# Performance work log

Hardware: AMD Instinct MI355X
Metric: run time of the kernel (lower is better)

The kernel has to match this reference:

```python
import jax, jax.numpy as jnp
import numpy as np

_B = 8      # number of graphs in batch
_H = 8      # attention heads
_GH = 64    # ProteinGraphConvModule output_dim / GRU hidden


def _custom_conv(x, src, dst, lw, lb, qw, qb, kw, kb, vw, vb, abias):
    # Per-edge multi-head attention: softmax is over the head axis within each edge
    n = x.shape[0]
    x = x @ lw + lb
    d = x.shape[1] // _H
    q = (x[dst] @ qw + qb).reshape(-1, _H, d)   # x_i = target nodes
    k = (x[src] @ kw + kb).reshape(-1, _H, d)   # x_j = source nodes
    v = (x[src] @ vw + vb).reshape(-1, _H, d)
    s = jnp.einsum('ehd,egd->ehg', q, k) * (1.0 / d ** 0.5) + abias[..., None]  # (E,H,H)
    a = jax.nn.softmax(s, axis=-1)
    out = jnp.einsum('ehg,egd->ehd', a, v).reshape(-1, _H * d)
    return jax.ops.segment_sum(out, dst, num_segments=n)  # aggr='add'


def _gcn(x, src, dst, w, b):
    # GCNConv: add self-loops + symmetric normalization
    n = x.shape[0]
    loop = jnp.arange(n)
    s = jnp.concatenate([src, loop])
    t = jnp.concatenate([dst, loop])
    deg = jax.ops.segment_sum(jnp.ones(s.shape[0], x.dtype), t, num_segments=n)
    dis = jnp.where(deg > 0, 1.0 / jnp.sqrt(deg), 0.0)
    h = x @ w
    msg = h[s] * (dis[s] * dis[t])[:, None]
    return jax.ops.segment_sum(msg, t, num_segments=n) + b


def _segment_mean(x, seg, nseg):
    ssum = jax.ops.segment_sum(x, seg, num_segments=nseg)
    cnt = jax.ops.segment_sum(jnp.ones(x.shape[0], x.dtype), seg, num_segments=nseg)
    return ssum / jnp.maximum(cnt, 1.0)[:, None]


def _pos_encoding(n, dim):
    pos = np.arange(n, dtype=np.float32)[:, None]
    div = np.exp(np.arange(0, dim, 2, dtype=np.float32) * (-np.log(10000.0) / dim))
    pe = np.zeros((n, dim), np.float32)
    pe[:, 0::2] = np.sin(pos * div)
    pe[:, 1::2] = np.cos(pos * div)
    return jnp.asarray(pe)


def _forward(x_wt, x_diff, emb_w, emb_b, cw_lin_w, cw_lin_b, cw_q_w, cw_q_b, cw_k_w, cw_k_b, cw_v_w, cw_v_b, cw_bias, c3_lin_w, c3_lin_b, c3_q_w, c3_q_b, c3_k_w, c3_k_b, c3_v_w, c3_v_b, c3_bias, sft_w, sft_b, gru_wih, gru_whh, gru_bih, gru_bhh, gcn_w1, gcn_b1, gcn_w2, gcn_b2, gcn_w3, gcn_b3, mlp_w1, mlp_b1, mlp_w2, mlp_b2, mlp_w3, mlp_b3, pred_w, pred_b, edge_index_wt, edge_index_diff, batch_wt, batch_diff):
    sw, dw = edge_index_wt[0], edge_index_wt[1]
    sd, dd = edge_index_diff[0], edge_index_diff[1]

    # ---- ProteinGraphConvModule ----
    x = jax.nn.relu(x_wt @ emb_w + emb_b)
    for i in range(2):  # GNN_depth-1 hidden CustomConvs
        x = jax.nn.relu(_custom_conv(x, sw, dw, cw_lin_w[i], cw_lin_b[i], cw_q_w[i], cw_q_b[i], cw_k_w[i], cw_k_b[i], cw_v_w[i], cw_v_b[i], cw_bias[i]))
    x = jax.nn.relu(_custom_conv(x, sw, dw, c3_lin_w, c3_lin_b, c3_q_w, c3_q_b, c3_k_w, c3_k_b, c3_v_w, c3_v_b, c3_bias))  # (N, 64)

    sf = _segment_mean(x, batch_wt, _B)
    sf = jax.nn.relu(sf @ sft_w + sft_b)
    # GRUCell with h0 = 0 (vectorized over batch)
    gi = sf @ gru_wih.T + gru_bih
    gh = jnp.zeros_like(sf) @ gru_whh.T + gru_bhh
    r = jax.nn.sigmoid(gi[:, :_GH] + gh[:, :_GH])
    z = jax.nn.sigmoid(gi[:, _GH:2 * _GH] + gh[:, _GH:2 * _GH])
    ng = jnp.tanh(gi[:, 2 * _GH:] + r * gh[:, 2 * _GH:])
    sf = (1.0 - z) * ng  # + z * h0 (h0=0)

    x = x + _pos_encoding(x.shape[0], _GH)
    vf_wt = jnp.concatenate([x, sf[batch_wt]], axis=1)  # (N, 128)

    # ---- DiffGraphGNN (eval mode: dropout = identity) ----
    y = jax.nn.relu(_gcn(x_diff, sd, dd, gcn_w1, gcn_b1))
    y = jax.nn.relu(_gcn(y, sd, dd, gcn_w2, gcn_b2))
    vf_diff = _gcn(y, sd, dd, gcn_w3, gcn_b3)  # (N, 128)

    # ---- Pool + MLP head ----
    g_wt = _segment_mean(vf_wt, batch_wt, _B)
    g_diff = _segment_mean(vf_diff, batch_diff, _B)
    h = jnp.concatenate([g_wt, g_diff], axis=-1)  # (B, 256)
    h = jax.nn.relu(h @ mlp_w1 + mlp_b1)
    h = jax.nn.relu(h @ mlp_w2 + mlp_b2)
    h = h @ mlp_w3 + mlp_b3
    return (h @ pred_w + pred_b).squeeze(-1)  # (B,)


def setup_inputs() -> dict:
    key = jax.random.key(0)
    ks = jax.random.split(key, 48)
    N, E, NF, HID = 6000, 200000, 64, 256
    inp = {}
    inp['x_wt'] = jax.random.normal(ks[0], (N, NF), jnp.float32)
    inp['x_diff'] = jax.random.normal(ks[1], (N, NF), jnp.float32)
    inp['edge_index_wt'] = jax.random.randint(ks[2], (2, E), 0, N)
    inp['edge_index_diff'] = jax.random.randint(ks[3], (2, E), 0, N)
    inp['batch_wt'] = jnp.sort(jax.random.randint(ks[4], (N,), 0, _B))
    inp['batch_diff'] = jnp.sort(jax.random.randint(ks[5], (N,), 0, _B))
    shapes = dict(
        emb_w=(NF, HID), emb_b=(HID,),
        cw_lin_w=(2, HID, HID), cw_lin_b=(2, HID), cw_q_w=(2, HID, HID), cw_q_b=(2, HID),
        cw_k_w=(2, HID, HID), cw_k_b=(2, HID), cw_v_w=(2, HID, HID), cw_v_b=(2, HID), cw_bias=(2, 1, _H),
        c3_lin_w=(HID, _GH), c3_lin_b=(_GH,), c3_q_w=(_GH, _GH), c3_q_b=(_GH,),
        c3_k_w=(_GH, _GH), c3_k_b=(_GH,), c3_v_w=(_GH, _GH), c3_v_b=(_GH,), c3_bias=(1, _H),
        sft_w=(_GH, _GH), sft_b=(_GH,),
        gru_wih=(3 * _GH, _GH), gru_whh=(3 * _GH, _GH), gru_bih=(3 * _GH,), gru_bhh=(3 * _GH,),
        gcn_w1=(NF, HID), gcn_b1=(HID,), gcn_w2=(HID, HID), gcn_b2=(HID,), gcn_w3=(HID, 128), gcn_b3=(128,),
        mlp_w1=(256, 128), mlp_b1=(128,), mlp_w2=(128, 128), mlp_b2=(128,), mlp_w3=(128, 128), mlp_b3=(128,),
        pred_w=(128, 1), pred_b=(1,))
    for j, (name, shp) in enumerate(shapes.items()):
        inp[name] = jax.random.normal(ks[6 + j], shp, jnp.float32) * 0.05
    return inp


def reference(x_wt, x_diff, emb_w, emb_b, cw_lin_w, cw_lin_b, cw_q_w, cw_q_b, cw_k_w, cw_k_b, cw_v_w, cw_v_b, cw_bias, c3_lin_w, c3_lin_b, c3_q_w, c3_q_b, c3_k_w, c3_k_b, c3_v_w, c3_v_b, c3_bias, sft_w, sft_b, gru_wih, gru_whh, gru_bih, gru_bhh, gcn_w1, gcn_b1, gcn_w2, gcn_b2, gcn_w3, gcn_b3, mlp_w1, mlp_b1, mlp_w2, mlp_b2, mlp_w3, mlp_b3, pred_w, pred_b, edge_index_wt, edge_index_diff, batch_wt, batch_diff):
    return _forward(x_wt, x_diff, emb_w, emb_b, cw_lin_w, cw_lin_b, cw_q_w, cw_q_b, cw_k_w, cw_k_b, cw_v_w, cw_v_b, cw_bias, c3_lin_w, c3_lin_b, c3_q_w, c3_q_b, c3_k_w, c3_k_b, c3_v_w, c3_v_b, c3_bias, sft_w, sft_b, gru_wih, gru_whh, gru_bih, gru_bhh, gcn_w1, gcn_b1, gcn_w2, gcn_b2, gcn_w3, gcn_b3, mlp_w1, mlp_b1, mlp_w2, mlp_b2, mlp_w3, mlp_b3, pred_w, pred_b, edge_index_wt, edge_index_diff, batch_wt, batch_diff)
```

## Files before the change

### kernel.cpp

```cpp
#include <hip/hip_runtime.h>
#include <hip/hip_bf16.h>


static inline int cdiv_h(int a, int b) { return (a + b - 1) / b; }

typedef __attribute__((ext_vector_type(8))) short bf16x8_t;
typedef __attribute__((ext_vector_type(4))) float f32x4_t;

__device__ __forceinline__ float bf16lo(uint32_t w) { return __uint_as_float(w << 16); }
__device__ __forceinline__ float bf16hi(uint32_t w) { return __uint_as_float(w & 0xffff0000u); }
__device__ __forceinline__ unsigned short f2bu(float f) {
  __hip_bfloat16 h = __float2bfloat16(f);
  return *reinterpret_cast<unsigned short*>(&h);
}
__device__ __forceinline__ uint32_t pk_bf16(float a, float b) {
  return (uint32_t)f2bu(a) | ((uint32_t)f2bu(b) << 16);
}

__global__ void fill_i2_kernel(int* __restrict__ a, int* __restrict__ b, int N) {
  int stride = gridDim.x * blockDim.x;
  for (int i = blockIdx.x * blockDim.x + threadIdx.x; i < 2 * N; i += stride) {
    if (i < N) a[i] = 0;
    else b[i - N] = 0;
  }
}

__global__ void hist2_kernel(const int* __restrict__ dst_a, int* __restrict__ deg_a,
                             const int* __restrict__ dst_b, int* __restrict__ deg_b, int E) {
  int i = blockIdx.x * blockDim.x + threadIdx.x;
  if (i < E) atomicAdd(&deg_a[dst_a[i]], 1);
  else if (i < 2 * E) atomicAdd(&deg_b[dst_b[i - E]], 1);
}

__global__ void scan2_kernel(int* __restrict__ cur_wt, int* __restrict__ rp_wt,
                             int* __restrict__ cur_df, int* __restrict__ rp_df,
                             float* __restrict__ dis, int N) {
  __shared__ int part[1024];
  const int g = blockIdx.x;
  int* deg = g ? cur_df : cur_wt;
  int* rowptr = g ? rp_df : rp_wt;
  const int t = threadIdx.x;
  const int chunk = (N + 1023) / 1024;
  const int base0 = t * chunk;
  int s = 0;
  for (int i = 0; i < chunk; ++i) {
    int idx = base0 + i;
    if (idx < N) s += deg[idx];
  }
  part[t] = s;
  __syncthreads();
  for (int off = 1; off < 1024; off <<= 1) {
    int v = (t >= off) ? part[t - off] : 0;
    __syncthreads();
    part[t] += v;
    __syncthreads();
  }
  int run = (t == 0) ? 0 : part[t - 1];
  for (int i = 0; i < chunk; ++i) {
    int idx = base0 + i;
    if (idx < N) {
      int d = deg[idx];
      rowptr[idx] = run;
      deg[idx] = run;
      if (g) dis[idx] = rsqrtf((float)d + 1.f);
      run += d;
    }
  }
  if (t == 1023) rowptr[N] = part[1023];
}

__global__ void fill_adj2_kernel(const int* __restrict__ src_a, const int* __restrict__ dst_a,
                                 int* __restrict__ cur_a, int* __restrict__ adj_a,
                                 const int* __restrict__ src_b, const int* __restrict__ dst_b,
                                 int* __restrict__ cur_b, int* __restrict__ adj_b, int E) {
  int i = blockIdx.x * blockDim.x + threadIdx.x;
  if (i < E) {
    int p = atomicAdd(&cur_a[dst_a[i]], 1);
    adj_a[p] = src_a[i];
  } else if (i < 2 * E) {
    int j = i - E;
    int p = atomicAdd(&cur_b[dst_b[j]], 1);
    adj_b[p] = src_b[j];
  }
}

__global__ void prep_inputs_kernel(const float* __restrict__ x_wt,
                                   const float* __restrict__ x_diff,
                                   const float* __restrict__ dis,
                                   __hip_bfloat16* __restrict__ xwtb,
                                   __hip_bfloat16* __restrict__ xd,
                                   float* __restrict__ seg, int n64) {
  int i = blockIdx.x * blockDim.x + threadIdx.x;
  if (i < n64) {
    xwtb[i] = __float2bfloat16(x_wt[i]);
  } else if (i < 2 * n64) {
    int j = i - n64;
    xd[j] = __float2bfloat16(x_diff[j] * dis[j >> 6]);
  } else if (i < 2 * n64 + 2064) {
    seg[i - 2 * n64] = 0.f;
  }
}

__global__ void transpose4_kernel(const float* __restrict__ emb_w, const float* __restrict__ w1,
                                  const float* __restrict__ w2, const float* __restrict__ w3,
                                  __hip_bfloat16* __restrict__ embT, __hip_bfloat16* __restrict__ w1T,
                                  __hip_bfloat16* __restrict__ w2T, __hip_bfloat16* __restrict__ w3T) {
  const int z = blockIdx.z;
  const float* W;
  __hip_bfloat16* WT;
  int K, N;
  if (z == 0) { W = emb_w; WT = embT; K = 64; N = 256; }
  else if (z == 1) { W = w1; WT = w1T; K = 64; N = 256; }
  else if (z == 2) { W = w2; WT = w2T; K = 256; N = 256; }
  else { W = w3; WT = w3T; K = 256; N = 128; }
  int idx = blockIdx.x * blockDim.x + threadIdx.x;
  if (idx < K * N) {
    int k = idx / N, n = idx % N;
    WT[(size_t)n * K + k] = __float2bfloat16(W[idx]);
  }
}

template <int KC, int EPI>
__device__ __forceinline__ void mfma_gemm_body(
    int rt, int cg, int z,
    const __hip_bfloat16* __restrict__ A, const __hip_bfloat16* __restrict__ WT,
    const float* __restrict__ bias, const float* __restrict__ rsc,
    float* __restrict__ outF, __hip_bfloat16* __restrict__ outB,
    int M, int N) {
  const int tid = threadIdx.x, w = tid >> 6, lane = tid & 63;
  const __hip_bfloat16* Wz = WT;
  const float* bz = bias;
  if (EPI >= 3) {
    Wz = WT + (size_t)z * KC * N;
    bz = bias + (size_t)z * N;
  }
  const int row0 = rt * 64;
  const int col0 = cg * 64 + w * 16;
  if (col0 >= N) return;
  const int r = lane & 15, kb = lane >> 4;
  f32x4_t acc[4];
#pragma unroll
  for (int i = 0; i < 4; ++i) acc[i] = (f32x4_t){0.f, 0.f, 0.f, 0.f};
  const __hip_bfloat16* bp = Wz + (size_t)(col0 + r) * KC + kb * 8;
  const __hip_bfloat16* ap[4];
#pragma unroll
  for (int i = 0; i < 4; ++i) {
    int rr = row0 + i * 16 + r;
    if (rr > M - 1) rr = M - 1;
    ap[i] = A + (size_t)rr * KC + kb * 8;
  }
#pragma unroll
  for (int k0 = 0; k0 < KC; k0 += 32) {
    bf16x8_t bv = *(const bf16x8_t*)(bp + k0);
#pragma unroll
    for (int i = 0; i < 4; ++i) {
      bf16x8_t av = *(const bf16x8_t*)(ap[i] + k0);
      acc[i] = __builtin_amdgcn_mfma_f32_16x16x32_bf16(av, bv, acc[i], 0, 0, 0);
    }
  }
  const int n = col0 + r;
#pragma unroll
  for (int i = 0; i < 4; ++i) {
#pragma unroll
    for (int j = 0; j < 4; ++j) {
      const int m = row0 + i * 16 + kb * 4 + j;
      if (m >= M) continue;
      float v = acc[i][j];
      if (EPI == 0) {
        v += bias[n];
        outB[(size_t)m * N + n] = __float2bfloat16(fmaxf(v, 0.f));
      } else if (EPI == 1) {
        v *= rsc[m];
        outB[(size_t)m * N + n] = __float2bfloat16(v);
      } else if (EPI == 3) {
        v += bz[n];
        if (z == 0)
          ((__hip_bfloat16*)outF)[(size_t)m * N + n] = __float2bfloat16(v);
        else if (z == 1)
          outB[(size_t)m * 2 * N + n] = __float2bfloat16(v);
        else
          outB[(size_t)m * 2 * N + N + (size_t)(n & 31) * 8 + (n >> 5)] = __float2bfloat16(v);
      } else {
        v += bz[n];
        if (z == 0)
          ((__hip_bfloat16*)outF)[(size_t)m * N + n] = __float2bfloat16(v);
        else if (z == 1)
          outB[(size_t)m * 2 * N + n] = __float2bfloat16(v);
        else
          outB[(size_t)m * 2 * N + N + (size_t)(n & 7) * 8 + (n >> 3)] = __float2bfloat16(v);
      }
    }
  }
}

__global__ void gemm_fold6_kernel(const float* __restrict__ lin_w, const float* __restrict__ qw,
                                  const float* __restrict__ kw, const float* __restrict__ vw,
                                  __hip_bfloat16* __restrict__ WfT) {
  const int z = blockIdx.z, l = z / 3, j = z % 3;
  const float* A = lin_w + (size_t)l * 65536;
  const float* W = ((j == 0) ? qw : (j == 1) ? kw : vw) + (size_t)l * 65536;
  __hip_bfloat16* C = WfT + (size_t)z * 65536;
  __shared__ float As[16][64];
  __shared__ float Bs[16][64];
  const int tx = threadIdx.x;
  const int m0 = blockIdx.x * 64, n0 = blockIdx.y * 64;
  const int tm = (tx & 15) * 4, tn = (tx >> 4) * 4;
  float acc[4][4] = {};
  for (int k0 = 0; k0 < 256; k0 += 16) {
    {
      int m = tx >> 2, kq = (tx & 3) * 4;
      float4 av = *(const float4*)(A + (size_t)(m0 + m) * 256 + (k0 + kq));
      As[kq + 0][m] = av.x; As[kq + 1][m] = av.y;
      As[kq + 2][m] = av.z; As[kq + 3][m] = av.w;
      int kk = tx >> 4, nq = (tx & 15) * 4;
      *(float4*)&Bs[kk][nq] = *(const float4*)(W + (size_t)(k0 + kk) * 256 + (n0 + nq));
    }
    __syncthreads();
#pragma unroll
    for (int k = 0; k < 16; ++k) {
      float4 a4 = *(const float4*)&As[k][tm];
      float4 b4 = *(const float4*)&Bs[k][tn];
      float av[4] = {a4.x, a4.y, a4.z, a4.w};
      float bv[4] = {b4.x, b4.y, b4.z, b4.w};
#pragma unroll
      for (int i = 0; i < 4; ++i)
#pragma unroll
        for (int j2 = 0; j2 < 4; ++j2) acc[i][j2] += av[i] * bv[j2];
    }
    __syncthreads();
  }
#pragma unroll
  for (int i = 0; i < 4; ++i)
#pragma unroll
    for (int j2 = 0; j2 < 4; ++j2)
      C[(size_t)(n0 + tn + j2) * 256 + (m0 + tm + i)] = __float2bfloat16(acc[i][j2]);
}

__global__ void gemm_fold3_kernel(const float* __restrict__ lin_w, const float* __restrict__ qw,
                                  const float* __restrict__ kw, const float* __restrict__ vw,
                                  __hip_bfloat16* __restrict__ WfT) {
  const int z = blockIdx.z;
  const float* A = lin_w;
  const float* W = (z == 0) ? qw : (z == 1) ? kw : vw;
  __hip_bfloat16* C = WfT + (size_t)z * 16384;
  __shared__ float As[16][64];
  __shared__ float Bs[16][64];
  const int tx = threadIdx.x;
  const int m0 = blockIdx.x * 64;
  const int tm = (tx & 15) * 4, tn = (tx >> 4) * 4;
  float acc[4][4] = {};
  for (int k0 = 0; k0 < 64; k0 += 16) {
    {
      int m = tx >> 2, kq = (tx & 3) * 4;
      float4 av = *(const float4*)(A + (size_t)(m0 + m) * 64 + (k0 + kq));
      As[kq + 0][m] = av.x; As[kq + 1][m] = av.y;
      As[kq + 2][m] = av.z; As[kq + 3][m] = av.w;
      int kk = tx >> 4, nq = (tx & 15) * 4;
      *(float4*)&Bs[kk][nq] = *(const float4*)(W + (size_t)(k0 + kk) * 64 + nq);
    }
    __syncthreads();
#pragma unroll
    for (int k = 0; k < 16; ++k) {
      float4 a4 = *(const float4*)&As[k][tm];
      float4 b4 = *(const float4*)&Bs[k][tn];
      float av[4] = {a4.x, a4.y, a4.z, a4.w};
      float bv[4] = {b4.x, b4.y, b4.z, b4.w};
#pragma unroll
      for (int i = 0; i < 4; ++i)
#pragma unroll
        for (int j2 = 0; j2 < 4; ++j2) acc[i][j2] += av[i] * bv[j2];
    }
    __syncthreads();
  }
#pragma unroll
  for (int i = 0; i < 4; ++i)
#pragma unroll
    for (int j2 = 0; j2 < 4; ++j2)
      C[(size_t)(tn + j2) * 256 + (m0 + tm + i)] = __float2bfloat16(acc[i][j2]);
}

__global__ void bias_fold9_kernel(const float* __restrict__ lin_b6, const float* __restrict__ qw6,
                                  const float* __restrict__ kw6, const float* __restrict__ vw6,
                                  const float* __restrict__ qb6, const float* __restrict__ kb6,
                                  const float* __restrict__ vb6, const float* __restrict__ lin_b3,
                                  const float* __restrict__ qw3, const float* __restrict__ kw3,
                                  const float* __restrict__ vw3, const float* __restrict__ qb3,
                                  const float* __restrict__ kb3, const float* __restrict__ vb3,
                                  float* __restrict__ bf6, float* __restrict__ bf3) {
  const int zb = blockIdx.x, c = threadIdx.x;
  if (zb < 6) {
    const int l = zb / 3, j = zb % 3;
    const float* W = ((j == 0) ? qw6 : (j == 1) ? kw6 : vw6) + (size_t)l * 65536;
    const float* b = ((j == 0) ? qb6 : (j == 1) ? kb6 : vb6) + l * 256;
    const float* lb = lin_b6 + l * 256;
    float acc = b[c];
    for (int k = 0; k < 256; ++k) acc += lb[k] * W[k * 256 + c];
    bf6[zb * 256 + c] = acc;
  } else if (c < 64) {
    const int j = zb - 6;
    const float* W = (j == 0) ? qw3 : (j == 1) ? kw3 : vw3;
    const float* b = (j == 0) ? qb3 : (j == 1) ? kb3 : vb3;
    float acc = b[c];
    for (int k = 0; k < 64; ++k) acc += lin_b3[k] * W[k * 64 + c];
    bf3[j * 64 + c] = acc;
  }
}

__device__ __forceinline__ void conv_mfma_body(
    int n, const __hip_bfloat16* __restrict__ Qn, const __hip_bfloat16* __restrict__ KV,
    const int* __restrict__ rowptr, const int* __restrict__ adj,
    const float* __restrict__ abias, __hip_bfloat16* __restrict__ Xout,
    float inv_sqrt_d) {
  __shared__ __align__(16) unsigned short sKV[4][2048];
  __shared__ __align__(16) unsigned short sP[4][640];
  __shared__ float sR[4][256];
  const int tid = threadIdx.x, w = tid >> 6, lane = tid & 63;
  const int c = lane & 15, kb = lane >> 4;

  const bf16x8_t qf = *(const bf16x8_t*)(Qn + (size_t)n * 256 + (size_t)(c & 7) * 32 + kb * 8);
  const float bh = abias[c & 7];

  unsigned short* myKV = sKV[w];
  unsigned short* myP = sP[w];
  f32x4_t acc0 = {0.f, 0.f, 0.f, 0.f};
  f32x4_t acc1 = {0.f, 0.f, 0.f, 0.f};
  const f32x4_t z4 = {0.f, 0.f, 0.f, 0.f};

  const int s0 = rowptr[n], t0 = rowptr[n + 1];
  auto ld = [&](int idx) -> uint4 {
    if (idx < t0) return *(const uint4*)(KV + (size_t)adj[idx] * 512 + (lane << 3));
    return make_uint4(0u, 0u, 0u, 0u);
  };
  int i = s0 + w * 4;
  uint4 kv0, kv1, kv2, kv3;
  if (i < t0) {
    kv0 = ld(i); kv1 = ld(i + 1); kv2 = ld(i + 2); kv3 = ld(i + 3);
  }
  for (; i < t0; i += 16) {
    *(uint4*)(myKV + 0 + (lane << 3)) = kv0;
    *(uint4*)(myKV + 512 + (lane << 3)) = kv1;
    *(uint4*)(myKV + 1024 + (lane << 3)) = kv2;
    *(uint4*)(myKV + 1536 + (lane << 3)) = kv3;
    const int i2 = i + 16;
    if (i2 < t0) {
      kv0 = ld(i2); kv1 = ld(i2 + 1); kv2 = ld(i2 + 2); kv3 = ld(i2 + 3);
    }
    __builtin_amdgcn_wave_barrier();
    const int aoff = (c >> 3) * 512 + (c & 7) * 32 + kb * 8;
    bf16x8_t a0 = *(const bf16x8_t*)(myKV + aoff);
    bf16x8_t a1 = *(const bf16x8_t*)(myKV + 1024 + aoff);
    f32x4_t S0 = __builtin_amdgcn_mfma_f32_16x16x32_bf16(a0, qf, z4, 0, 0, 0);
    f32x4_t S1 = __builtin_amdgcn_mfma_f32_16x16x32_bf16(a1, qf, z4, 0, 0, 0);
    float p0[4], p1[4];
    {
      float sv[4];
#pragma unroll
      for (int j = 0; j < 4; ++j) sv[j] = S0[j] * inv_sqrt_d + bh;
      float m = fmaxf(fmaxf(sv[0], sv[1]), fmaxf(sv[2], sv[3]));
      m = fmaxf(m, __shfl_xor(m, 16));
      float sum = 0.f;
#pragma unroll
      for (int j = 0; j < 4; ++j) { p0[j] = __expf(sv[j] - m); sum += p0[j]; }
      sum += __shfl_xor(sum, 16);
      float rs = 1.f / sum;
#pragma unroll
      for (int j = 0; j < 4; ++j) p0[j] *= rs;
    }
    {
      float sv[4];
#pragma unroll
      for (int j = 0; j < 4; ++j) sv[j] = S1[j] * inv_sqrt_d + bh;
      float m = fmaxf(fmaxf(sv[0], sv[1]), fmaxf(sv[2], sv[3]));
      m = fmaxf(m, __shfl_xor(m, 16));
      float sum = 0.f;
#pragma unroll
      for (int j = 0; j < 4; ++j) { p1[j] = __expf(sv[j] - m); sum += p1[j]; }
      sum += __shfl_xor(sum, 16);
      float rs = 1.f / sum;
#pragma unroll
      for (int j = 0; j < 4; ++j) p1[j] *= rs;
    }
    *(uint32_t*)(myP + c * 40 + kb * 4) = pk_bf16(p0[0], p0[1]);
    *(uint32_t*)(myP + c * 40 + kb * 4 + 2) = pk_bf16(p0[2], p0[3]);
    *(uint32_t*)(myP + c * 40 + 16 + kb * 4) = pk_bf16(p1[0], p1[1]);
    *(uint32_t*)(myP + c * 40 + 16 + kb * 4 + 2) = pk_bf16(p1[2], p1[3]);
    __builtin_amdgcn_wave_barrier();
    bf16x8_t pa = *(const bf16x8_t*)(myP + c * 40 + kb * 8);
    bf16x8_t vb0 = *(const bf16x8_t*)(myKV + kb * 512 + 256 + c * 8);
    bf16x8_t vb1 = *(const bf16x8_t*)(myKV + kb * 512 + 256 + (c + 16) * 8);
    acc0 = __builtin_amdgcn_mfma_f32_16x16x32_bf16(pa, vb0, acc0, 0, 0, 0);
    acc1 = __builtin_amdgcn_mfma_f32_16x16x32_bf16(pa, vb1, acc1, 0, 0, 0);
    __builtin_amdgcn_wave_barrier();
  }
  if (kb < 2) {
#pragma unroll
    for (int j = 0; j < 4; ++j) {
      int h = kb * 4 + j;
      sR[w][h * 32 + c] = acc0[j];
      sR[w][h * 32 + 16 + c] = acc1[j];
    }
  }
  __syncthreads();
  for (int cc = tid; cc < 256; cc += 256) {
    float v = sR[0][cc] + sR[1][cc] + sR[2][cc] + sR[3][cc];
    Xout[(size_t)n * 256 + cc] = __float2bfloat16(fmaxf(v, 0.f));
  }
}

__device__ __forceinline__ void conv3_mfma_body(
    int n, const __hip_bfloat16* __restrict__ Qn, const __hip_bfloat16* __restrict__ KV,
    const int* __restrict__ rowptr, const int* __restrict__ adj,
    const float* __restrict__ abias, float* __restrict__ Xout, float inv_sqrt_d) {
  __shared__ __align__(16) unsigned short sKV3[4][544];
  __shared__ __align__(16) unsigned short sP3[4][320];
  __shared__ float sR3[4][64];
  const int tid = threadIdx.x, w = tid >> 6, lane = tid & 63;
  const int c = lane & 15, kb = lane >> 4;

  bf16x8_t qf = {};
  if (kb == 0) qf = *(const bf16x8_t*)(Qn + (size_t)n * 64 + (size_t)(c & 7) * 8);
  const float bh = abias[c & 7];

  unsigned short* myKV = sKV3[w];
  unsigned short* myP = sP3[w];
  f32x4_t acc = {0.f, 0.f, 0.f, 0.f};
  const f32x4_t z4 = {0.f, 0.f, 0.f, 0.f};

  const int s0 = rowptr[n], t0 = rowptr[n + 1];
  auto ld = [&](int idx) -> uint4 {
    if (idx < t0) return *(const uint4*)(KV + (size_t)adj[idx] * 128 + (c << 3));
    return make_uint4(0u, 0u, 0u, 0u);
  };
  int i = s0 + w * 4;
  uint4 kvst = make_uint4(0u, 0u, 0u, 0u);
  if (i < t0) kvst = ld(i + kb);
  for (; i < t0; i += 16) {
    *(uint4*)(myKV + kb * 136 + (c << 3)) = kvst;
    kvst = ld(i + 16 + kb);
    __builtin_amdgcn_wave_barrier();
    bf16x8_t a0 = {}, a1 = {};
    if (kb == 0) {
      a0 = *(const bf16x8_t*)(myKV + (c >> 3) * 136 + (c & 7) * 8);
      a1 = *(const bf16x8_t*)(myKV + (2 + (c >> 3)) * 136 + (c & 7) * 8);
    }
    f32x4_t S0 = __builtin_amdgcn_mfma_f32_16x16x32_bf16(a0, qf, z4, 0, 0, 0);
    f32x4_t S1 = __builtin_amdgcn_mfma_f32_16x16x32_bf16(a1, qf, z4, 0, 0, 0);
    float p0[4], p1[4];
    {
      float sv[4];
#pragma unroll
      for (int j = 0; j < 4; ++j) sv[j] = S0[j] * inv_sqrt_d + bh;
      float m = fmaxf(fmaxf(sv[0], sv[1]), fmaxf(sv[2], sv[3]));
      m = fmaxf(m, __shfl_xor(m, 16));
      float sum = 0.f;
#pragma unroll
      for (int j = 0; j < 4; ++j) { p0[j] = __expf(sv[j] - m); sum += p0[j]; }
      sum += __shfl_xor(sum, 16);
      float rs = 1.f / sum;
#pragma unroll
      for (int j = 0; j < 4; ++j) p0[j] *= rs;
    }
    {
      float sv[4];
#pragma unroll
      for (int j = 0; j < 4; ++j) sv[j] = S1[j] * inv_sqrt_d + bh;
      float m = fmaxf(fmaxf(sv[0], sv[1]), fmaxf(sv[2], sv[3]));
      m = fmaxf(m, __shfl_xor(m, 16));
      float sum = 0.f;
#pragma unroll
      for (int j = 0; j < 4; ++j) { p1[j] = __expf(sv[j] - m); sum += p1[j]; }
      sum += __shfl_xor(sum, 16);
      float rs = 1.f / sum;
#pragma unroll
      for (int j = 0; j < 4; ++j) p1[j] *= rs;
    }
    if (c < 8) {
      const int k0 = (kb >> 1) * 8 + (kb & 1) * 4;
      *(uint32_t*)(myP + c * 40 + k0) = pk_bf16(p0[0], p0[1]);
      *(uint32_t*)(myP + c * 40 + k0 + 2) = pk_bf16(p0[2], p0[3]);
      *(uint32_t*)(myP + c * 40 + 16 + k0) = pk_bf16(p1[0], p1[1]);
      *(uint32_t*)(myP + c * 40 + 16 + k0 + 2) = pk_bf16(p1[2], p1[3]);
    }
    __builtin_amdgcn_wave_barrier();
    bf16x8_t pa = *(const bf16x8_t*)(myP + (c & 7) * 40 + kb * 8);
    bf16x8_t vb = {};
    if (c < 8) vb = *(const bf16x8_t*)(myKV + kb * 136 + 64 + c * 8);
    acc = __builtin_amdgcn_mfma_f32_16x16x32_bf16(pa, vb, acc, 0, 0, 0);
    __builtin_amdgcn_wave_barrier();
  }
  if (kb < 2 && c < 8) {
#pragma unroll
    for (int j = 0; j < 4; ++j) sR3[w][(kb * 4 + j) * 8 + c] = acc[j];
  }
  __syncthreads();
  if (tid < 64) {
    float v = sR3[0][tid] + sR3[1][tid] + sR3[2][tid] + sR3[3][tid];
    Xout[(size_t)n * 64 + tid] = fmaxf(v, 0.f);
  }
}

template <int C, bool BIAS, bool RELU, bool OBF>
__device__ __forceinline__ void gcn_gather_body(
    int n, const __hip_bfloat16* __restrict__ Hd, const int* __restrict__ rowptr,
    const int* __restrict__ adj, const float* __restrict__ dis,
    const float* __restrict__ bias, void* __restrict__ O) {
  constexpr int EPL = C / 64;
  __shared__ float sRG[4][C];
  const int tid = threadIdx.x, w = tid >> 6, lane = tid & 63;
  float acc[EPL] = {};
  const int s = rowptr[n], t = rowptr[n + 1];
  int i = s + w;
  int vs = (i < t) ? adj[i] : 0;
  if constexpr (EPL == 4) {
    uint2 u = (i < t) ? *(const uint2*)(Hd + (size_t)vs * C + lane * 4) : make_uint2(0u, 0u);
    while (i < t) {
      const int i2 = i + 4;
      const int vs2 = (i2 < t) ? adj[i2] : 0;
      uint2 un = (i2 < t) ? *(const uint2*)(Hd + (size_t)vs2 * C + lane * 4) : make_uint2(0u, 0u);
      acc[0] += bf16lo(u.x); acc[1] += bf16hi(u.x);
      acc[2] += bf16lo(u.y); acc[3] += bf16hi(u.y);
      u = un; i = i2; vs = vs2;
    }
  } else if constexpr (EPL == 2) {
    uint32_t u = (i < t) ? *(const uint32_t*)(Hd + (size_t)vs * C + lane * 2) : 0u;
    while (i < t) {
      const int i2 = i + 4;
      const int vs2 = (i2 < t) ? adj[i2] : 0;
      uint32_t un = (i2 < t) ? *(const uint32_t*)(Hd + (size_t)vs2 * C + lane * 2) : 0u;
      acc[0] += bf16lo(u); acc[1] += bf16hi(u);
      u = un; i = i2; vs = vs2;
    }
  } else {
    unsigned short u = (i < t) ? *(const unsigned short*)(Hd + (size_t)vs * C + lane) : 0;
    while (i < t) {
      const int i2 = i + 4;
      const int vs2 = (i2 < t) ? adj[i2] : 0;
      unsigned short un = (i2 < t) ? *(const unsigned short*)(Hd + (size_t)vs2 * C + lane) : 0;
      acc[0] += bf16lo((uint32_t)u);
      u = un; i = i2; vs = vs2;
    }
  }
  if (w == 0) {
    const __hip_bfloat16* hn = Hd + (size_t)n * C;
#pragma unroll
    for (int j = 0; j < EPL; ++j)
      acc[j] += bf16lo((uint32_t)*(const unsigned short*)(hn + lane * EPL + j));
  }
#pragma unroll
  for (int j = 0; j < EPL; ++j) sRG[w][lane * EPL + j] = acc[j];
  __syncthreads();
  const float dn = dis[n];
  for (int c = tid; c < C; c += 256) {
    float v = (sRG[0][c] + sRG[1][c] + sRG[2][c] + sRG[3][c]) * dn;
    if (BIAS) v += bias[c];
    if (RELU) v = fmaxf(v, 0.f);
    if (OBF)
      ((__hip_bfloat16*)O)[(size_t)n * C + c] = __float2bfloat16(v);
    else
      ((float*)O)[(size_t)n * C + c] = v;
  }
}

__device__ __forceinline__ void segsum_vfd_body(
    int bid, int nb, const float* __restrict__ VFD, const int* __restrict__ batch,
    float* __restrict__ sum_vfd, float* __restrict__ cnt, int N) {
  __shared__ float lv[1024], lc[8];
  const int tid = threadIdx.x;
  for (int i = tid; i < 1024; i += 256) lv[i] = 0.f;
  if (tid < 8) lc[tid] = 0.f;
  __syncthreads();
  const int stride = nb * 256;
  for (int i = bid * 256 + tid; i < N * 128; i += stride) {
    int n = i >> 7, c = i & 127;
    int b = batch[n];
    atomicAdd(&lv[(b << 7) + c], VFD[i]);
    if (c == 0) atomicAdd(&lc[b], 1.f);
  }
  __syncthreads();
  for (int j = tid; j < 1024; j += 256) {
    if (lv[j] != 0.f) atomicAdd(&sum_vfd[j], lv[j]);
  }
  if (tid < 8 && lc[tid] != 0.f) atomicAdd(&cnt[tid], lc[tid]);
}

__global__ void segsum_x3_pe_kernel(const float* __restrict__ X3, const int* __restrict__ batch,
                                    float* __restrict__ sum_x3, float* __restrict__ sum_pe,
                                    float* __restrict__ cnt, int N) {
  __shared__ float lx[512], lp[512], lc[8];
  const int tid = threadIdx.x;
  for (int i = tid; i < 512; i += 256) { lx[i] = 0.f; lp[i] = 0.f; }
  if (tid < 8) lc[tid] = 0.f;
  __syncthreads();
  const int stride = gridDim.x * 256;
  for (int i = blockIdx.x * 256 + tid; i < N * 64; i += stride) {
    int n = i >> 6, c = i & 63;
    int b = batch[n];
    atomicAdd(&lx[(b << 6) + c], X3[i]);
    const float F = -0.14391156831f;
    float arg = (float)n * __expf(F * (float)(c & ~1));
    atomicAdd(&lp[(b << 6) + c], (c & 1) ? __cosf(arg) : __sinf(arg));
    if (c == 0) atomicAdd(&lc[b], 1.f);
  }
  __syncthreads();
  for (int j = tid; j < 512; j += 256) {
    if (lx[j] != 0.f) atomicAdd(&sum_x3[j], lx[j]);
    if (lp[j] != 0.f) atomicAdd(&sum_pe[j], lp[j]);
  }
  if (tid < 8 && lc[tid] != 0.f) atomicAdd(&cnt[tid], lc[tid]);
}

__global__ __launch_bounds__(256) void m1_kernel(
    const __hip_bfloat16* Hd1, const int* rp_df, const int* adj_df, const float* dis,
    __hip_bfloat16* G1,
    const __hip_bfloat16* xwtb, const __hip_bfloat16* embT, const float* emb_b,
    __hip_bfloat16* Xb, int Nn, int NB) {
  if ((int)blockIdx.x < NB) {
    gcn_gather_body<64, false, false, true>(blockIdx.x, Hd1, rp_df, adj_df, dis, nullptr, G1);
  } else {
    int g = blockIdx.x - NB;
    mfma_gemm_body<64, 0>(g >> 2, g & 3, 0, xwtb, embT, emb_b, nullptr, nullptr, Xb, Nn, 256);
  }
}

__global__ __launch_bounds__(256) void m2_kernel(
    const __hip_bfloat16* G1, const __hip_bfloat16* w1T, const float* gcn_b1,
    __hip_bfloat16* Y1,
    const __hip_bfloat16* Xb, const __hip_bfloat16* WfT, const float* bf,
    __hip_bfloat16* Q16, __hip_bfloat16* KV, int Nn, int pz) {
  if ((int)blockIdx.x < pz) {
    int g = blockIdx.x;
    mfma_gemm_body<64, 0>(g >> 2, g & 3, 0, G1, w1T, gcn_b1, nullptr, nullptr, Y1, Nn, 256);
  } else {
    int q = blockIdx.x - pz;
    int z = q / pz, rem = q % pz;
    mfma_gemm_body<256, 3>(rem >> 2, rem & 3, z, Xb, WfT, bf, nullptr, (float*)Q16, KV,
                           Nn, 256);
  }
}

__global__ __launch_bounds__(256) void m3_kernel(
    const __hip_bfloat16* Q16, const __hip_bfloat16* KV, const int* rp_wt,
    const int* adj_wt, const float* abias, __hip_bfloat16* Xb, float isd,
    const __hip_bfloat16* Y1, const __hip_bfloat16* w2T, const float* dis,
    __hip_bfloat16* Hd2, int Nn, int NB) {
  if ((int)blockIdx.x < NB) {
    conv_mfma_body(blockIdx.x, Q16, KV, rp_wt, adj_wt, abias, Xb, isd);
  } else {
    int g = blockIdx.x - NB;
    mfma_gemm_body<256, 1>(g >> 2, g & 3, 0, Y1, w2T, nullptr, dis, nullptr, Hd2, Nn, 256);
  }
}

__global__ __launch_bounds__(256) void m4_kernel(
    const __hip_bfloat16* Xb, const __hip_bfloat16* WfT, const float* bf,
    __hip_bfloat16* Q16, __hip_bfloat16* KV,
    const __hip_bfloat16* Hd2, const int* rp_df, const int* adj_df, const float* dis,
    const float* gcn_b2, __hip_bfloat16* Y2b, int Nn, int pz) {
  const int nq = pz * 3;
  if ((int)blockIdx.x < nq) {
    int q = blockIdx.x;
    int z = q / pz, rem = q % pz;
    mfma_gemm_body<256, 3>(rem >> 2, rem & 3, z, Xb, WfT, bf, nullptr, (float*)Q16, KV,
                           Nn, 256);
  } else {
    gcn_gather_body<256, true, true, true>(blockIdx.x - nq, Hd2, rp_df, adj_df, dis,
                                           gcn_b2, Y2b);
  }
}

__global__ __launch_bounds__(256) void m5_kernel(
    const __hip_bfloat16* Q16, const __hip_bfloat16* KV, const int* rp_wt,
    const int* adj_wt, const float* abias, __hip_bfloat16* Xb, float isd,
    const __hip_bfloat16* Y2b, const __hip_bfloat16* w3T, const float* dis,
    __hip_bfloat16* Hd3, int Nn, int NB) {
  if ((int)blockIdx.x < NB) {
    conv_mfma_body(blockIdx.x, Q16, KV, rp_wt, adj_wt, abias, Xb, isd);
  } else {
    int g = blockIdx.x - NB;
    mfma_gemm_body<256, 1>(g >> 1, g & 1, 0, Y2b, w3T, nullptr, dis, nullptr, Hd3, Nn, 128);
  }
}

__global__ __launch_bounds__(256) void m6_kernel(
    const __hip_bfloat16* Xb, const __hip_bfloat16* Wf3T, const float* bf3,
    __hip_bfloat16* Q16, __hip_bfloat16* KV,
    const __hip_bfloat16* Hd3, const int* rp_df, const int* adj_df, const float* dis,
    const float* gcn_b3, float* VFD, int Nn, int mt) {
  const int nq = mt * 3;
  if ((int)blockIdx.x < nq) {
    int q = blockIdx.x;
    int z = q / mt, row = q % mt;
    mfma_gemm_body<256, 4>(row, 0, z, Xb, Wf3T, bf3, nullptr, (float*)Q16, KV, Nn, 64);
  } else {
    gcn_gather_body<128, true, false, false>(blockIdx.x - nq, Hd3, rp_df, adj_df, dis,
                                             gcn_b3, VFD);
  }
}

__global__ __launch_bounds__(256) void m7_kernel(
    const __hip_bfloat16* Q16, const __hip_bfloat16* KV, const int* rp_wt,
    const int* adj_wt, const float* c3_bias, float* X3, float isd,
    const float* VFD, const int* b_df, float* sum_vfd, float* cnt_df, int Nn, int NB) {
  if ((int)blockIdx.x < NB) {
    conv3_mfma_body(blockIdx.x, Q16, KV, rp_wt, adj_wt, c3_bias, X3, isd);
  } else {
    segsum_vfd_body(blockIdx.x - NB, 120, VFD, b_df, sum_vfd, cnt_df, Nn);
  }
}

__global__ __launch_bounds__(256) void head_kernel(
    const float* __restrict__ sum_x3, const float* __restrict__ sum_pe,
    const float* __restrict__ cnt_wt, const float* __restrict__ sum_vfd,
    const float* __restrict__ cnt_df, const float* __restrict__ sft_w,
    const float* __restrict__ sft_b, const float* __restrict__ gru_wih,
    const float* __restrict__ gru_bih, const float* __restrict__ gru_bhh,
    const float* __restrict__ mlp_w1, const float* __restrict__ mlp_b1,
    const float* __restrict__ mlp_w2, const float* __restrict__ mlp_b2,
    const float* __restrict__ mlp_w3, const float* __restrict__ mlp_b3,
    const float* __restrict__ pred_w, const float* __restrict__ pred_b,
    float* __restrict__ out) {
  const int b = blockIdx.x;
  const int tid = threadIdx.x;
  __shared__ float sf0[64], sf1[64], sfr[64];
  __shared__ float hcat[256];
  __shared__ float m1[128], m2[128], m3[128];
  __shared__ float part4[4][64];
  __shared__ float part2[2][128];
  __shared__ float gi[192];
  __shared__ float rsum[4];

  const float cw = fmaxf(cnt_wt[b], 1.f), cd = fmaxf(cnt_df[b], 1.f);
  if (tid < 64) sf0[tid] = sum_x3[(b << 6) + tid] / cw;
  __syncthreads();
  {
    const int c = tid & 63, q = tid >> 6;
    float acc = 0.f;
#pragma unroll
    for (int k = q * 16; k < q * 16 + 16; ++k) acc += sf0[k] * sft_w[k * 64 + c];
    part4[q][c] = acc;
  }
  __syncthreads();
  if (tid < 64)
    sf1[tid] = fmaxf(part4[0][tid] + part4[1][tid] + part4[2][tid] + part4[3][tid] +
                         sft_b[tid], 0.f);
  __syncthreads();
  if (tid < 192) {
    float acc = gru_bih[tid];
    const float* wr = gru_wih + tid * 64;
#pragma unroll 8
    for (int k = 0; k < 64; ++k) acc += sf1[k] * wr[k];
    gi[tid] = acc;
  }
  __syncthreads();
  if (tid < 64) {
    float r = 1.f / (1.f + __expf(-(gi[tid] + gru_bhh[tid])));
    float z = 1.f / (1.f + __expf(-(gi[64 + tid] + gru_bhh[64 + tid])));
    float ng = tanhf(gi[128 + tid] + r * gru_bhh[128 + tid]);
    sfr[tid] = (1.f - z) * ng;
  }
  __syncthreads();
  {
    const int c = tid;
    float v;
    if (c < 64)
      v = (sum_x3[(b << 6) + c] + sum_pe[(b << 6) + c]) / cw;
    else if (c < 128)
      v = sfr[c - 64];
    else
      v = sum_vfd[(b << 7) + (c - 128)] / cd;
    hcat[c] = v;
  }
  __syncthreads();
  {
    const int c = tid & 127, h = tid >> 7;
    float acc = 0.f;
#pragma unroll 8
    for (int k = h * 128; k < h * 128 + 128; ++k) acc += hcat[k] * mlp_w1[k * 128 + c];
    part2[h][c] = acc;
  }
  __syncthreads();
  if (tid < 128) m1[tid] = fmaxf(part2[0][tid] + part2[1][tid] + mlp_b1[tid], 0.f);
  __syncthreads();
  {
    const int c = tid & 127, h = tid >> 7;
    float acc = 0.f;
#pragma unroll 8
    for (int k = h * 64; k < h * 64 + 64; ++k) acc += m1[k] * mlp_w2[k * 128 + c];
    part2[h][c] = acc;
  }
  __syncthreads();
  if (tid < 128) m2[tid] = fmaxf(part2[0][tid] + part2[1][tid] + mlp_b2[tid], 0.f);
  __syncthreads();
  {
    const int c = tid & 127, h = tid >> 7;
    float acc = 0.f;
#pragma unroll 8
    for (int k = h * 64; k < h * 64 + 64; ++k) acc += m2[k] * mlp_w3[k * 128 + c];
    part2[h][c] = acc;
  }
  __syncthreads();
  if (tid < 128) m3[tid] = part2[0][tid] + part2[1][tid] + mlp_b3[tid];
  __syncthreads();
  if (tid < 128) {
    float p = m3[tid] * pred_w[tid];
    p += __shfl_down(p, 32);
    p += __shfl_down(p, 16);
    p += __shfl_down(p, 8);
    p += __shfl_down(p, 4);
    p += __shfl_down(p, 2);
    p += __shfl_down(p, 1);
    if ((tid & 63) == 0) rsum[tid >> 6] = p;
  }
  __syncthreads();
  if (tid == 0) out[b] = rsum[0] + rsum[1] + pred_b[0];
}

extern "C" void kernel_launch(void* const* d_in, const int* in_sizes, int n_in,
                              void* d_out, int out_size, void* d_ws, size_t ws_size,
                              hipStream_t stream) {
  const float* x_wt = (const float*)d_in[0];
  const float* x_diff = (const float*)d_in[1];
  const int* ei_wt = (const int*)d_in[2];
  const int* ei_df = (const int*)d_in[3];
  const int* b_wt = (const int*)d_in[4];
  const int* b_df = (const int*)d_in[5];
  const float* emb_w = (const float*)d_in[6];
  const float* emb_b = (const float*)d_in[7];
  const float* cw_lin_w = (const float*)d_in[8];
  const float* cw_lin_b = (const float*)d_in[9];
  const float* cw_q_w = (const float*)d_in[10];
  const float* cw_q_b = (const float*)d_in[11];
  const float* cw_k_w = (const float*)d_in[12];
  const float* cw_k_b = (const float*)d_in[13];
  const float* cw_v_w = (const float*)d_in[14];
  const float* cw_v_b = (const float*)d_in[15];
  const float* cw_bias = (const float*)d_in[16];
  const float* c3_lin_w = (const float*)d_in[17];
  const float* c3_lin_b = (const float*)d_in[18];
  const float* c3_q_w = (const float*)d_in[19];
  const float* c3_q_b = (const float*)d_in[20];
  const float* c3_k_w = (const float*)d_in[21];
  const float* c3_k_b = (const float*)d_in[22];
  const float* c3_v_w = (const float*)d_in[23];
  const float* c3_v_b = (const float*)d_in[24];
  const float* c3_bias = (const float*)d_in[25];
  const float* sft_w = (const float*)d_in[26];
  const float* sft_b = (const float*)d_in[27];
  const float* gru_wih = (const float*)d_in[28];
  const float* gru_bih = (const float*)d_in[30];
  const float* gru_bhh = (const float*)d_in[31];
  const float* gcn_w1 = (const float*)d_in[32];
  const float* gcn_b1 = (const float*)d_in[33];
  const float* gcn_w2 = (const float*)d_in[34];
  const float* gcn_b2 = (const float*)d_in[35];
  const float* gcn_w3 = (const float*)d_in[36];
  const float* gcn_b3 = (const float*)d_in[37];
  const float* mlp_w1 = (const float*)d_in[38];
  const float* mlp_b1 = (const float*)d_in[39];
  const float* mlp_w2 = (const float*)d_in[40];
  const float* mlp_b2 = (const float*)d_in[41];
  const float* mlp_w3 = (const float*)d_in[42];
  const float* mlp_b3 = (const float*)d_in[43];
  const float* pred_w = (const float*)d_in[44];
  const float* pred_b = (const float*)d_in[45];

  const int N = in_sizes[0] / 64;
  const int E = in_sizes[2] / 2;
  const int* src_wt = ei_wt;
  const int* dst_wt = ei_wt + E;
  const int* src_df = ei_df;
  const int* dst_df = ei_df + E;

  float* ws = (float*)d_ws;
  const size_t fN256 = (size_t)N * 256;
  float* X = ws;
  float* L = ws + 1 * fN256;
  float* Qb = ws + 2 * fN256;
  float* Kb = ws + 3 * fN256;
  float* Vb = ws + 4 * fN256;
  float* X3 = ws + 5 * fN256;
  float* DIS = X3 + (size_t)N * 64;
  float* SEG = DIS + (((size_t)N + 63) / 64) * 64;
  float* sum_x3 = SEG;
  float* sum_pe = SEG + 512;
  float* cnt_wt = SEG + 1024;
  float* sum_vfd = SEG + 1032;
  float* cnt_df = SEG + 2056;
  int* ip = (int*)(SEG + 2064 + 16);
  int* rp_wt = ip;
  int* cur_wt = rp_wt + (N + 1);
  int* adj_wt = cur_wt + N;
  int* rp_df = adj_wt + E;
  int* cur_df = rp_df + (N + 1);
  int* adj_df = cur_df + N;
  __hip_bfloat16* wb = (__hip_bfloat16*)((((uintptr_t)(adj_df + E)) + 63) & ~(uintptr_t)63);
  __hip_bfloat16* WfT6 = wb;
  __hip_bfloat16* Wf3T = WfT6 + 6 * 65536;
  __hip_bfloat16* embT = Wf3T + 3 * 16384;
  __hip_bfloat16* w1T = embT + 16384;
  __hip_bfloat16* w2T = w1T + 16384;
  __hip_bfloat16* w3T = w2T + 65536;
  __hip_bfloat16* Hd1 = w3T + 32768;
  float* bf6 = (float*)((((uintptr_t)(Hd1 + (size_t)N * 64)) + 63) & ~(uintptr_t)63);
  float* bf3 = bf6 + 6 * 256;

  __hip_bfloat16* Xb = (__hip_bfloat16*)X;
  __hip_bfloat16* xwtb = (__hip_bfloat16*)L;
  __hip_bfloat16* Y1 = (__hip_bfloat16*)L;
  __hip_bfloat16* Y2b = (__hip_bfloat16*)L;
  float* VFD = L;
  __hip_bfloat16* Qb16 = (__hip_bfloat16*)Qb;
  __hip_bfloat16* KVb = (__hip_bfloat16*)Kb;
  __hip_bfloat16* G1 = (__hip_bfloat16*)Vb;
  __hip_bfloat16* Hd2 = (__hip_bfloat16*)Vb;
  __hip_bfloat16* Hd3 = (__hip_bfloat16*)Vb;

  const int TB = 256;
  const int MT64 = cdiv_h(N, 64);
  const int PZ = MT64 * 4;

  gemm_fold6_kernel<<<dim3(4, 4, 6), TB, 0, stream>>>(cw_lin_w, cw_q_w, cw_k_w, cw_v_w, WfT6);
  gemm_fold3_kernel<<<dim3(4, 1, 3), TB, 0, stream>>>(c3_lin_w, c3_q_w, c3_k_w, c3_v_w, Wf3T);
  bias_fold9_kernel<<<9, TB, 0, stream>>>(cw_lin_b, cw_q_w, cw_k_w, cw_v_w, cw_q_b, cw_k_b,
                                          cw_v_b, c3_lin_b, c3_q_w, c3_k_w, c3_v_w, c3_q_b,
                                          c3_k_b, c3_v_b, bf6, bf3);
  transpose4_kernel<<<dim3(256, 1, 4), TB, 0, stream>>>(emb_w, gcn_w1, gcn_w2, gcn_w3,
                                                        embT, w1T, w2T, w3T);

  fill_i2_kernel<<<48, TB, 0, stream>>>(cur_wt, cur_df, N);
  hist2_kernel<<<cdiv_h(2 * E, TB), TB, 0, stream>>>(dst_wt, cur_wt, dst_df, cur_df, E);
  scan2_kernel<<<2, 1024, 0, stream>>>(cur_wt, rp_wt, cur_df, rp_df, DIS, N);
  fill_adj2_kernel<<<cdiv_h(2 * E, TB), TB, 0, stream>>>(src_wt, dst_wt, cur_wt, adj_wt,
                                                         src_df, dst_df, cur_df, adj_df, E);

  prep_inputs_kernel<<<cdiv_h(2 * N * 64 + 2064, TB), TB, 0, stream>>>(
      x_wt, x_diff, DIS, xwtb, Hd1, SEG, N * 64);

  const float isd32 = 0.17677669529663687f;
  const float isd8 = 0.35355339059327373f;

  m1_kernel<<<N + PZ, TB, 0, stream>>>(Hd1, rp_df, adj_df, DIS, G1, xwtb, embT, emb_b,
                                       Xb, N, N);
  m2_kernel<<<PZ + PZ * 3, TB, 0, stream>>>(G1, w1T, gcn_b1, Y1, Xb, WfT6, bf6,
                                            Qb16, KVb, N, PZ);
  m3_kernel<<<N + PZ, TB, 0, stream>>>(Qb16, KVb, rp_wt, adj_wt, cw_bias, Xb, isd32,
                                       Y1, w2T, DIS, Hd2, N, N);
  m4_kernel<<<PZ * 3 + N, TB, 0, stream>>>(Xb, WfT6 + (size_t)3 * 65536, bf6 + 768,
                                           Qb16, KVb, Hd2, rp_df, adj_df, DIS, gcn_b2,
                                           Y2b, N, PZ);
  m5_kernel<<<N + MT64 * 2, TB, 0, stream>>>(Qb16, KVb, rp_wt, adj_wt, cw_bias + 8, Xb,
                                             isd32, Y2b, w3T, DIS, Hd3, N, N);
  m6_kernel<<<MT64 * 3 + N, TB, 0, stream>>>(Xb, Wf3T, bf3, Qb16, KVb, Hd3, rp_df,
                                             adj_df, DIS, gcn_b3, VFD, N, MT64);
  m7_kernel<<<N + 120, TB, 0, stream>>>(Qb16, KVb, rp_wt, adj_wt, c3_bias, X3, isd8,
                                        VFD, b_df, sum_vfd, cnt_df, N, N);

  segsum_x3_pe_kernel<<<120, TB, 0, stream>>>(X3, b_wt, sum_x3, sum_pe, cnt_wt, N);

  head_kernel<<<8, TB, 0, stream>>>(sum_x3, sum_pe, cnt_wt, sum_vfd, cnt_df, sft_w, sft_b,
                                    gru_wih, gru_bih, gru_bhh, mlp_w1, mlp_b1, mlp_w2,
                                    mlp_b2, mlp_w3, mlp_b3, pred_w, pred_b, (float*)d_out);
}
```

Baseline: 361.6 us.

## Assign one wave per node in attention conv kernels instead of one block

The conv attention bodies used to spread each node's edges over four waves and reduce their partial results through shared memory with a block barrier. Each wave now owns a whole node, walks all of that node's edges in steps of four, and writes its output directly. This removes the LDS reduction and the __syncthreads, and the grid shrinks to a quarter of the conv blocks. In exchange, each node's edge loop runs serially in one wave, so per-wave latency grows for high-degree nodes and load balance depends on the degree distribution.

```diff
diff --git a/kernel.cpp b/kernel.cpp
--- a/kernel.cpp
+++ b/kernel.cpp
@@ -313,7 +313,6 @@
     float inv_sqrt_d) {
   __shared__ __align__(16) unsigned short sKV[4][2048];
   __shared__ __align__(16) unsigned short sP[4][640];
-  __shared__ float sR[4][256];
   const int tid = threadIdx.x, w = tid >> 6, lane = tid & 63;
   const int c = lane & 15, kb = lane >> 4;
 
@@ -331,17 +330,17 @@
     if (idx < t0) return *(const uint4*)(KV + (size_t)adj[idx] * 512 + (lane << 3));
     return make_uint4(0u, 0u, 0u, 0u);
   };
-  int i = s0 + w * 4;
+  int i = s0;
   uint4 kv0, kv1, kv2, kv3;
   if (i < t0) {
     kv0 = ld(i); kv1 = ld(i + 1); kv2 = ld(i + 2); kv3 = ld(i + 3);
   }
-  for (; i < t0; i += 16) {
+  for (; i < t0; i += 4) {
     *(uint4*)(myKV + 0 + (lane << 3)) = kv0;
     *(uint4*)(myKV + 512 + (lane << 3)) = kv1;
     *(uint4*)(myKV + 1024 + (lane << 3)) = kv2;
     *(uint4*)(myKV + 1536 + (lane << 3)) = kv3;
-    const int i2 = i + 16;
+    const int i2 = i + 4;
     if (i2 < t0) {
       kv0 = ld(i2); kv1 = ld(i2 + 1); kv2 = ld(i2 + 2); kv3 = ld(i2 + 3);
     }
@@ -396,14 +395,9 @@
 #pragma unroll
     for (int j = 0; j < 4; ++j) {
       int h = kb * 4 + j;
-      sR[w][h * 32 + c] = acc0[j];
-      sR[w][h * 32 + 16 + c] = acc1[j];
-    }
-  }
-  __syncthreads();
-  for (int cc = tid; cc < 256; cc += 256) {
-    float v = sR[0][cc] + sR[1][cc] + sR[2][cc] + sR[3][cc];
-    Xout[(size_t)n * 256 + cc] = __float2bfloat16(fmaxf(v, 0.f));
+      Xout[(size_t)n * 256 + h * 32 + c] = __float2bfloat16(fmaxf(acc0[j], 0.f));
+      Xout[(size_t)n * 256 + h * 32 + 16 + c] = __float2bfloat16(fmaxf(acc1[j], 0.f));
+    }
   }
 }
 
@@ -413,7 +407,6 @@
     const float* __restrict__ abias, float* __restrict__ Xout, float inv_sqrt_d) {
   __shared__ __align__(16) unsigned short sKV3[4][544];
   __shared__ __align__(16) unsigned short sP3[4][320];
-  __shared__ float sR3[4][64];
   const int tid = threadIdx.x, w = tid >> 6, lane = tid & 63;
   const int c = lane & 15, kb = lane >> 4;
 
@@ -431,12 +424,12 @@
     if (idx < t0) return *(const uint4*)(KV + (size_t)adj[idx] * 128 + (c << 3));
     return make_uint4(0u, 0u, 0u, 0u);
   };
-  int i = s0 + w * 4;
+  int i = s0;
   uint4 kvst = make_uint4(0u, 0u, 0u, 0u);
   if (i < t0) kvst = ld(i + kb);
-  for (; i < t0; i += 16) {
+  for (; i < t0; i += 4) {
     *(uint4*)(myKV + kb * 136 + (c << 3)) = kvst;
-    kvst = ld(i + 16 + kb);
+    kvst = ld(i + 4 + kb);
     __builtin_amdgcn_wave_barrier();
     bf16x8_t a0 = {}, a1 = {};
     if (kb == 0) {
@@ -490,12 +483,8 @@
   }
   if (kb < 2 && c < 8) {
 #pragma unroll
-    for (int j = 0; j < 4; ++j) sR3[w][(kb * 4 + j) * 8 + c] = acc[j];
-  }
-  __syncthreads();
-  if (tid < 64) {
-    float v = sR3[0][tid] + sR3[1][tid] + sR3[2][tid] + sR3[3][tid];
-    Xout[(size_t)n * 64 + tid] = fmaxf(v, 0.f);
+    for (int j = 0; j < 4; ++j)
+      Xout[(size_t)n * 64 + (kb * 4 + j) * 8 + c] = fmaxf(acc[j], 0.f);
   }
 }
 
@@ -642,11 +631,12 @@
     const __hip_bfloat16* Q16, const __hip_bfloat16* KV, const int* rp_wt,
     const int* adj_wt, const float* abias, __hip_bfloat16* Xb, float isd,
     const __hip_bfloat16* Y1, const __hip_bfloat16* w2T, const float* dis,
-    __hip_bfloat16* Hd2, int Nn, int NB) {
-  if ((int)blockIdx.x < NB) {
-    conv_mfma_body(blockIdx.x, Q16, KV, rp_wt, adj_wt, abias, Xb, isd);
+    __hip_bfloat16* Hd2, int Nn, int NB4) {
+  if ((int)blockIdx.x < NB4) {
+    int n = blockIdx.x * 4 + (threadIdx.x >> 6);
+    if (n < Nn) conv_mfma_body(n, Q16, KV, rp_wt, adj_wt, abias, Xb, isd);
   } else {
-    int g = blockIdx.x - NB;
+    int g = blockIdx.x - NB4;
     mfma_gemm_body<256, 1>(g >> 2, g & 3, 0, Y1, w2T, nullptr, dis, nullptr, Hd2, Nn, 256);
   }
 }
@@ -672,11 +662,12 @@
     const __hip_bfloat16* Q16, const __hip_bfloat16* KV, const int* rp_wt,
     const int* adj_wt, const float* abias, __hip_bfloat16* Xb, float isd,
     const __hip_bfloat16* Y2b, const __hip_bfloat16* w3T, const float* dis,
-    __hip_bfloat16* Hd3, int Nn, int NB) {
-  if ((int)blockIdx.x < NB) {
-    conv_mfma_body(blockIdx.x, Q16, KV, rp_wt, adj_wt, abias, Xb, isd);
+    __hip_bfloat16* Hd3, int Nn, int NB4) {
+  if ((int)blockIdx.x < NB4) {
+    int n = blockIdx.x * 4 + (threadIdx.x >> 6);
+    if (n < Nn) conv_mfma_body(n, Q16, KV, rp_wt, adj_wt, abias, Xb, isd);
   } else {
-    int g = blockIdx.x - NB;
+    int g = blockIdx.x - NB4;
     mfma_gemm_body<256, 1>(g >> 1, g & 1, 0, Y2b, w3T, nullptr, dis, nullptr, Hd3, Nn, 128);
   }
 }
@@ -700,11 +691,12 @@
 __global__ __launch_bounds__(256) void m7_kernel(
     const __hip_bfloat16* Q16, const __hip_bfloat16* KV, const int* rp_wt,
     const int* adj_wt, const float* c3_bias, float* X3, float isd,
-    const float* VFD, const int* b_df, float* sum_vfd, float* cnt_df, int Nn, int NB) {
-  if ((int)blockIdx.x < NB) {
-    conv3_mfma_body(blockIdx.x, Q16, KV, rp_wt, adj_wt, c3_bias, X3, isd);
+    const float* VFD, const int* b_df, float* sum_vfd, float* cnt_df, int Nn, int NB4) {
+  if ((int)blockIdx.x < NB4) {
+    int n = blockIdx.x * 4 + (threadIdx.x >> 6);
+    if (n < Nn) conv3_mfma_body(n, Q16, KV, rp_wt, adj_wt, c3_bias, X3, isd);
   } else {
-    segsum_vfd_body(blockIdx.x - NB, 120, VFD, b_df, sum_vfd, cnt_df, Nn);
+    segsum_vfd_body(blockIdx.x - NB4, 120, VFD, b_df, sum_vfd, cnt_df, Nn);
   }
 }
 
@@ -918,6 +910,7 @@
   const int TB = 256;
   const int MT64 = cdiv_h(N, 64);
   const int PZ = MT64 * 4;
+  const int NB4 = cdiv_h(N, 4);
 
   gemm_fold6_kernel<<<dim3(4, 4, 6), TB, 0, stream>>>(cw_lin_w, cw_q_w, cw_k_w, cw_v_w, WfT6);
   gemm_fold3_kernel<<<dim3(4, 1, 3), TB, 0, stream>>>(c3_lin_w, c3_q_w, c3_k_w, c3_v_w, Wf3T);
@@ -943,17 +936,17 @@
                                        Xb, N, N);
   m2_kernel<<<PZ + PZ * 3, TB, 0, stream>>>(G1, w1T, gcn_b1, Y1, Xb, WfT6, bf6,
                                             Qb16, KVb, N, PZ);
-  m3_kernel<<<N + PZ, TB, 0, stream>>>(Qb16, KVb, rp_wt, adj_wt, cw_bias, Xb, isd32,
-                                       Y1, w2T, DIS, Hd2, N, N);
+  m3_kernel<<<NB4 + PZ, TB, 0, stream>>>(Qb16, KVb, rp_wt, adj_wt, cw_bias, Xb, isd32,
+                                         Y1, w2T, DIS, Hd2, N, NB4);
   m4_kernel<<<PZ * 3 + N, TB, 0, stream>>>(Xb, WfT6 + (size_t)3 * 65536, bf6 + 768,
                                            Qb16, KVb, Hd2, rp_df, adj_df, DIS, gcn_b2,
                                            Y2b, N, PZ);
-  m5_kernel<<<N + MT64 * 2, TB, 0, stream>>>(Qb16, KVb, rp_wt, adj_wt, cw_bias + 8, Xb,
-                                             isd32, Y2b, w3T, DIS, Hd3, N, N);
+  m5_kernel<<<NB4 + MT64 * 2, TB, 0, stream>>>(Qb16, KVb, rp_wt, adj_wt, cw_bias + 8, Xb,
+                                               isd32, Y2b, w3T, DIS, Hd3, N, NB4);
   m6_kernel<<<MT64 * 3 + N, TB, 0, stream>>>(Xb, Wf3T, bf3, Qb16, KVb, Hd3, rp_df,
                                              adj_df, DIS, gcn_b3, VFD, N, MT64);
-  m7_kernel<<<N + 120, TB, 0, stream>>>(Qb16, KVb, rp_wt, adj_wt, c3_bias, X3, isd8,
-                                        VFD, b_df, sum_vfd, cnt_df, N, N);
+  m7_kernel<<<NB4 + 120, TB, 0, stream>>>(Qb16, KVb, rp_wt, adj_wt, c3_bias, X3, isd8,
+                                          VFD, b_df, sum_vfd, cnt_df, N, NB4);
 
   segsum_x3_pe_kernel<<<120, TB, 0, stream>>>(X3, b_wt, sum_x3, sum_pe, cnt_wt, N);
 
```

Result: faster. 339.6 us (-6.1%).
